# Kernel tuning notes

Hardware: AMD Instinct MI355X
Metric: run time of the kernel (lower is better)

## Reference

```python
import jax, jax.numpy as jnp
import numpy as np
import math

D_MODEL = 768
N_HEAD = 12
HEAD_DIM = D_MODEL // N_HEAD
B = 4
W = 32
HW = W * W


def setup_inputs() -> dict:
    key = jax.random.key(0)
    k1, k2, k3 = jax.random.split(key, 3)
    x = jax.random.normal(k1, (B, HW, D_MODEL), dtype=jnp.float32)
    w_qkv = jax.random.normal(k2, (3 * D_MODEL, D_MODEL), dtype=jnp.float32) * (D_MODEL ** -0.5)
    w_out = jax.random.normal(k3, (D_MODEL, D_MODEL), dtype=jnp.float32) * (D_MODEL ** -0.5)
    gamma = jnp.ones((D_MODEL,), dtype=jnp.float32)
    return {"x": x, "w_qkv": w_qkv, "w_out": w_out, "gamma": gamma}


def _axial_sincos(w, head_dim, dtype):
    # Axial RoPE: first half of head_dim encodes row position, second half column.
    dim_half = head_dim // 2
    inv_freq = 1.0 / (10000.0 ** (jnp.arange(0, dim_half, 2, dtype=dtype) / dim_half))  # (dim_half//2,)
    pos = jnp.arange(w, dtype=dtype)
    ang = pos[:, None] * inv_freq[None, :]                 # (w, f)
    row = jnp.repeat(ang[:, None, :], w, axis=1)           # (w, w, f)
    col = jnp.repeat(ang[None, :, :], w, axis=0)           # (w, w, f)
    theta = jnp.concatenate([row, col], axis=-1).reshape(w * w, dim_half)  # (hw, head_dim//2)
    theta = jnp.concatenate([theta, theta], axis=-1)       # rotate-half layout -> (hw, head_dim)
    return jnp.sin(theta), jnp.cos(theta)


def _rotate_half(t):
    t1, t2 = jnp.split(t, 2, axis=-1)
    return jnp.concatenate([-t2, t1], axis=-1)


def _apply_rotary(t, sin, cos):
    return t * cos + _rotate_half(t) * sin


def _rms_norm(x, gamma, eps=1e-6):
    return x * jax.lax.rsqrt(jnp.mean(x * x, axis=-1, keepdims=True) + eps) * gamma


def _attn_mask(w):
    # Faithful to the torch source: mask[center, neighbor] = False, else True.
    # torch SDPA bool semantics: True = attend. So 3x3 neighbors are EXCLUDED.
    idx = jnp.arange(w * w)
    r, c = idx // w, idx % w
    neighbor = (jnp.abs(r[:, None] - r[None, :]) <= 1) & (jnp.abs(c[:, None] - c[None, :]) <= 1)
    return ~neighbor  # (hw, hw) bool, True = allowed


def reference(x, w_qkv, w_out, gamma):
    Bx, hw, d = x.shape
    w = int(math.isqrt(hw))
    h, hd = N_HEAD, HEAD_DIM
    sin, cos = _axial_sincos(w, hd, x.dtype)               # (hw, hd) each
    xn = _rms_norm(x, gamma)
    qkv = xn @ w_qkv.T                                     # (B, hw, 3d)
    qkv = qkv.reshape(Bx, hw, 3, h, hd)
    q = jnp.transpose(qkv[:, :, 0], (0, 2, 1, 3))          # (B, h, hw, hd)
    k = jnp.transpose(qkv[:, :, 1], (0, 2, 1, 3))
    v = jnp.transpose(qkv[:, :, 2], (0, 2, 1, 3))
    q = _apply_rotary(q, sin, cos)
    k = _apply_rotary(k, sin, cos)
    allow = _attn_mask(w)
    scale = 1.0 / jnp.sqrt(jnp.asarray(hd, x.dtype))
    scores = jnp.einsum('bhid,bhjd->bhij', q, k) * scale   # (B, h, hw, hw)
    scores = jnp.where(allow[None, None], scores, jnp.asarray(-jnp.inf, x.dtype))
    probs = jax.nn.softmax(scores, axis=-1)
    out = jnp.einsum('bhij,bhjd->bhid', probs, v)          # (B, h, hw, hd)
    out = jnp.transpose(out, (0, 2, 1, 3)).reshape(Bx, hw, d)
    return out @ w_out.T
```

## Files before the change

### kernel.cpp

```cpp
#include <hip/hip_runtime.h>

typedef __attribute__((ext_vector_type(8))) short short8;
typedef __attribute__((ext_vector_type(4))) float f32x4;
typedef __attribute__((ext_vector_type(4))) unsigned short ushort4_t;
typedef unsigned short ushort_t;
typedef unsigned long long u64;

#define D_MODEL 768
#define NHEAD 12
#define HD 64
#define BATCH 4
#define HWIDTH 32
#define HW 1024
#define TOK (BATCH*HW)
#define QKV_N (3*D_MODEL)
#define BH (BATCH*NHEAD)
#define QSCALE 0.18033688f

__device__ __forceinline__ ushort_t f2bf(float f) {
    union { float f; unsigned u; } v; v.f = f;
    unsigned u = v.u;
    unsigned r = u + 0x7FFFu + ((u >> 16) & 1u);
    return (ushort_t)(r >> 16);
}
__device__ __forceinline__ float bf2f(ushort_t h) {
    union { unsigned u; float f; } v; v.u = ((unsigned)h) << 16;
    return v.f;
}
__device__ __forceinline__ float ex2(float x) {
    float r; asm("v_exp_f32 %0, %1" : "=v"(r) : "v"(x)); return r;
}
__device__ __forceinline__ unsigned cvtpk(float lo, float hi) {
    unsigned r; asm("v_cvt_pk_bf16_f32 %0, %1, %2" : "=v"(r) : "v"(lo), "v"(hi)); return r;
}

__global__ void rmsnorm_kernel(const float* __restrict__ x, const float* __restrict__ gamma,
                               ushort_t* __restrict__ xn) {
    int wave = threadIdx.x >> 6, lane = threadIdx.x & 63;
    int t = blockIdx.x * 4 + wave;
    const float* xr = x + (size_t)t * D_MODEL;
    float v[12]; float ss = 0.f;
    #pragma unroll
    for (int j = 0; j < 12; ++j) { v[j] = xr[lane + j*64]; ss += v[j]*v[j]; }
    #pragma unroll
    for (int m = 1; m < 64; m <<= 1) ss += __shfl_xor(ss, m, 64);
    float r = rsqrtf(ss * (1.f/768.f) + 1e-6f);
    ushort_t* o = xn + (size_t)t * D_MODEL;
    #pragma unroll
    for (int j = 0; j < 12; ++j) o[lane + j*64] = f2bf(v[j] * r * gamma[lane + j*64]);
}

__global__ void cvt_kernel(const float* __restrict__ in, ushort_t* __restrict__ out, int n) {
    int i = blockIdx.x * blockDim.x + threadIdx.x;
    if (i < n) out[i] = f2bf(in[i]);
}

__global__ void sincos_kernel(float* __restrict__ sint, float* __restrict__ cost) {
    int i = blockIdx.x * blockDim.x + threadIdx.x;
    int p = i >> 5, j = i & 31;
    int r = p >> 5, c = p & 31;
    int jj = j & 15;
    float freq = powf(10000.f, -(float)(2*jj) / 32.f);
    float pos = (j < 16) ? (float)r : (float)c;
    float th = pos * freq;
    sint[i] = sinf(th);
    cost[i] = cosf(th);
}

template<int NTILES, int EPI>
__global__ __launch_bounds__(256, 2) void gemm128(const ushort_t* __restrict__ A,
                                                  const ushort_t* __restrict__ B,
                                                  const float* __restrict__ sint,
                                                  const float* __restrict__ cost,
                                                  ushort_t* __restrict__ Qr,
                                                  ushort_t* __restrict__ Kr,
                                                  ushort_t* __restrict__ VTt,
                                                  float* __restrict__ C) {
    __shared__ ushort_t As[2][128*64];
    __shared__ ushort_t Bs[2][128*64];
    const int K = 768;
    constexpr int NR = NTILES / 2;
    int c = blockIdx.x & 7;
    int l = blockIdx.x >> 3;
    int mtile = (c >> 1)*8 + l / NR;
    int ntile = (c & 1)*NR + l % NR;
    int tm = mtile * 128, tn = ntile * 128;
    int w = threadIdx.x >> 6, lane = threadIdx.x & 63;
    int wr = w >> 1, wc = w & 1;
    int l15 = lane & 15, l4 = lane >> 4;

    const ushort_t* mat = (w < 2) ? A : B;
    int mbase = (w < 2) ? tm : tn;
    ushort_t* lds_half = (w < 2) ? &As[0][0] : &Bs[0][0];
    int r0w = (w & 1) * 64;
    int srow = r0w + (lane >> 3);
    int sslot = (lane & 7) ^ (srow & 7);
    const ushort_t* gsrc0 = mat + (size_t)(mbase + srow)*K + sslot*8;

    auto stage = [&](int buf, int kstep) {
        int k0 = kstep * 64;
        #pragma unroll
        for (int j = 0; j < 8; ++j) {
            const ushort_t* g = gsrc0 + (size_t)(j*8)*K + k0;
            __builtin_amdgcn_global_load_lds((const __attribute__((address_space(1))) void*)g,
                (__attribute__((address_space(3))) void*)(lds_half + (size_t)buf*8192 + (r0w + j*8)*64),
                16, 0, 0);
        }
    };

    f32x4 acc[4][4] = {};
    auto compute = [&](int bi) {
        short8 af[4][2], bfx[4][2];
        #pragma unroll
        for (int mi = 0; mi < 4; ++mi) {
            int row = wr*64 + mi*16 + l15;
            #pragma unroll
            for (int kk = 0; kk < 2; ++kk)
                af[mi][kk] = *(const short8*)&As[bi][row*64 + ((kk*4 + l4) ^ (row & 7))*8];
        }
        #pragma unroll
        for (int ni = 0; ni < 4; ++ni) {
            int row = wc*64 + ni*16 + l15;
            #pragma unroll
            for (int kk = 0; kk < 2; ++kk)
                bfx[ni][kk] = *(const short8*)&Bs[bi][row*64 + ((kk*4 + l4) ^ (row & 7))*8];
        }
        #pragma unroll
        for (int kk = 0; kk < 2; ++kk)
            #pragma unroll
            for (int mi = 0; mi < 4; ++mi)
                #pragma unroll
                for (int ni = 0; ni < 4; ++ni)
                    acc[mi][ni] = __builtin_amdgcn_mfma_f32_16x16x32_bf16(af[mi][kk], bfx[ni][kk], acc[mi][ni], 0, 0, 0);
    };

    stage(0, 0); stage(1, 1);
    for (int t = 0; t < 12; ++t) {
        if (t < 11) { asm volatile("s_waitcnt vmcnt(8)" ::: "memory"); }
        else        { asm volatile("s_waitcnt vmcnt(0)" ::: "memory"); }
        __builtin_amdgcn_s_barrier();
        compute(t & 1);
        __builtin_amdgcn_s_barrier();
        if (t < 10) stage(t & 1, t + 2);
    }

    if constexpr (EPI == 0) {
        int col_base = tn + wc*64;
        int region = col_base / 768;
        int h = (col_base % 768) >> 6;
        if (region < 2) {
            ushort_t* dst = (region == 0) ? Qr : Kr;
            float scale = (region == 0) ? QSCALE : 1.f;
            #pragma unroll
            for (int mi = 0; mi < 4; ++mi) {
                #pragma unroll
                for (int ni = 0; ni < 2; ++ni) {
                    int d = ni*16 + l15;
                    #pragma unroll
                    for (int r = 0; r < 4; ++r) {
                        int pt = tm + wr*64 + mi*16 + l4*4 + r;
                        int b = pt >> 10, p = pt & 1023;
                        float s = sint[p*32 + d], cc = cost[p*32 + d];
                        float t0 = acc[mi][ni][r], t1 = acc[mi][ni+2][r];
                        size_t o = (size_t)(b*NHEAD + h)*HW*HD + (size_t)p*HD + d;
                        dst[o]      = f2bf((t0*cc - t1*s) * scale);
                        dst[o + 32] = f2bf((t1*cc + t0*s) * scale);
                    }
                }
            }
        } else {
            #pragma unroll
            for (int mi = 0; mi < 4; ++mi) {
                int pt = tm + wr*64 + mi*16 + l4*4;
                int b = pt >> 10, p = pt & 1023;
                size_t hb = (size_t)(b*NHEAD + h)*HD*HW;
                #pragma unroll
                for (int ni = 0; ni < 4; ++ni) {
                    int d = ni*16 + l15;
                    ushort4_t pk;
                    pk.x = f2bf(acc[mi][ni][0]);
                    pk.y = f2bf(acc[mi][ni][1]);
                    pk.z = f2bf(acc[mi][ni][2]);
                    pk.w = f2bf(acc[mi][ni][3]);
                    *(ushort4_t*)&VTt[hb + (size_t)d*HW + p] = pk;
                }
            }
        }
    } else {
        #pragma unroll
        for (int mi = 0; mi < 4; ++mi)
            #pragma unroll
            for (int ni = 0; ni < 4; ++ni)
                #pragma unroll
                for (int r = 0; r < 4; ++r) {
                    int row = tm + wr*64 + mi*16 + l4*4 + r;
                    int col = tn + wc*64 + ni*16 + l15;
                    C[(size_t)row*(128*NTILES) + col] = acc[mi][ni][r];
                }
    }
}

__global__ __launch_bounds__(256) void attn_kernel(const ushort_t* __restrict__ Q,
                                                   const ushort_t* __restrict__ Kt,
                                                   const ushort_t* __restrict__ VT,
                                                   ushort_t* __restrict__ Ao) {
    __shared__ ushort_t Kb[2][64*64];
    __shared__ ushort_t Vb[2][64*64];
    __shared__ ushort_t P[4][16][72];
    int flat = blockIdx.x;
    int swz = (flat & 7) * 96 + (flat >> 3);
    int bh = swz >> 4;
    int qtile = swz & 15;
    int w = threadIdx.x >> 6, lane = threadIdx.x & 63;
    int l15 = lane & 15, l4 = lane >> 4;
    int qbase = qtile * 64 + w * 16;
    int q = qbase + l15;
    int qr = q >> 5, qc = q & 31;
    const ushort_t* Qh = Q + (size_t)bh * HW * HD;
    const ushort_t* Kh = Kt + (size_t)bh * HW * HD;
    const ushort_t* Vh = VT + (size_t)bh * HD * HW;
    short8 aq0 = *(const short8*)&Qh[(size_t)q*64 + l4*8];
    short8 aq1 = *(const short8*)&Qh[(size_t)q*64 + 32 + l4*8];
    unsigned pat = (qc == 0) ? 3u : (7u << (qc - 1));
    float m = -1e30f, lsum = 0.f;
    f32x4 oacc[4] = {};

    auto stage = [&](int bufi, int kv) {
        #pragma unroll
        for (int is = 0; is < 2; ++is) {
            int c = is*256 + w*64 + lane;
            int row = c >> 3;
            int col16 = (c & 7) ^ (row & 7);
            const ushort_t* ga = Kh + (size_t)(kv + row)*64 + col16*8;
            __builtin_amdgcn_global_load_lds((const __attribute__((address_space(1))) void*)ga,
                (__attribute__((address_space(3))) void*)(&Kb[bufi][(size_t)(is*256 + w*64)*8]), 16, 0, 0);
            const ushort_t* gv = Vh + (size_t)row*HW + kv + col16*8;
            __builtin_amdgcn_global_load_lds((const __attribute__((address_space(1))) void*)gv,
                (__attribute__((address_space(3))) void*)(&Vb[bufi][(size_t)(is*256 + w*64)*8]), 16, 0, 0);
        }
    };

    stage(0, 0); stage(1, 64);

    for (int t = 0; t < 16; ++t) {
        if (t < 15) { asm volatile("s_waitcnt vmcnt(4)" ::: "memory"); }
        else        { asm volatile("s_waitcnt vmcnt(0)" ::: "memory"); }
        __builtin_amdgcn_s_barrier();
        int cur = t & 1;
        int kv = t * 64;
        int sw = l15 & 7;
        f32x4 s[4];
        #pragma unroll
        for (int st = 0; st < 4; ++st) {
            int krow = st*16 + l15;
            short8 bk0 = *(const short8*)&Kb[cur][(size_t)krow*64 + (size_t)((l4 ^ sw))*8];
            short8 bk1 = *(const short8*)&Kb[cur][(size_t)krow*64 + (size_t)(((4+l4) ^ sw))*8];
            f32x4 z = {};
            z = __builtin_amdgcn_mfma_f32_16x16x32_bf16(bk0, aq0, z, 0, 0, 0);
            z = __builtin_amdgcn_mfma_f32_16x16x32_bf16(bk1, aq1, z, 0, 0, 0);
            s[st] = z;
        }
        short8 va0[4], va1[4];
        #pragma unroll
        for (int dt = 0; dt < 4; ++dt) {
            int vrow = dt*16 + l15;
            va0[dt] = *(const short8*)&Vb[cur][(size_t)vrow*64 + (size_t)((l4 ^ sw))*8];
            va1[dt] = *(const short8*)&Vb[cur][(size_t)vrow*64 + (size_t)(((4+l4) ^ sw))*8];
        }
        int dr = qr - (kv >> 5);
        if (dr >= -1 && dr <= 2) {
            u64 tm = 0;
            if (dr <= 1) tm |= (u64)pat;
            if (dr >= 0) tm |= ((u64)pat) << 32;
            u64 sub = tm >> (l4*4);
            #pragma unroll
            for (int st = 0; st < 4; ++st)
                #pragma unroll
                for (int i = 0; i < 4; ++i)
                    if ((sub >> (st*16 + i)) & 1) s[st][i] = -1e30f;
        }
        float vmax = fmaxf(
            fmaxf(fmaxf(fmaxf(s[0][0], s[0][1]), fmaxf(s[0][2], s[0][3])),
                  fmaxf(fmaxf(s[1][0], s[1][1]), fmaxf(s[1][2], s[1][3]))),
            fmaxf(fmaxf(fmaxf(s[2][0], s[2][1]), fmaxf(s[2][2], s[2][3])),
                  fmaxf(fmaxf(s[3][0], s[3][1]), fmaxf(s[3][2], s[3][3]))));
        vmax = fmaxf(vmax, __shfl_xor(vmax, 16, 64));
        vmax = fmaxf(vmax, __shfl_xor(vmax, 32, 64));
        if (__any(vmax - m > 8.f)) {
            float mn = fmaxf(m, vmax);
            float sf = ex2(m - mn);
            lsum *= sf;
            #pragma unroll
            for (int dt = 0; dt < 4; ++dt)
                #pragma unroll
                for (int i = 0; i < 4; ++i) oacc[dt][i] *= sf;
            m = mn;
        }
        float ls = 0.f;
        #pragma unroll
        for (int st = 0; st < 4; ++st) {
            float p0 = ex2(s[st][0] - m), p1 = ex2(s[st][1] - m);
            float p2 = ex2(s[st][2] - m), p3 = ex2(s[st][3] - m);
            ls += (p0 + p1) + (p2 + p3);
            uint2 pk;
            pk.x = cvtpk(p0, p1);
            pk.y = cvtpk(p2, p3);
            *(uint2*)&P[w][l15][st*16 + l4*4] = pk;
        }
        ls += __shfl_xor(ls, 16, 64);
        ls += __shfl_xor(ls, 32, 64);
        lsum += ls;
        short8 pf0 = *(const short8*)&P[w][l15][l4*8];
        short8 pf1 = *(const short8*)&P[w][l15][32 + l4*8];
        #pragma unroll
        for (int dt = 0; dt < 4; ++dt) {
            oacc[dt] = __builtin_amdgcn_mfma_f32_16x16x32_bf16(va0[dt], pf0, oacc[dt], 0, 0, 0);
            oacc[dt] = __builtin_amdgcn_mfma_f32_16x16x32_bf16(va1[dt], pf1, oacc[dt], 0, 0, 0);
        }
        __builtin_amdgcn_s_barrier();
        if (t < 14) stage(cur, (t + 2) * 64);
    }
    int b = bh / NHEAD, h = bh % NHEAD;
    float rl = 1.f / lsum;
    size_t obase = ((size_t)b*HW + q)*D_MODEL + h*64;
    #pragma unroll
    for (int dt = 0; dt < 4; ++dt) {
        uint2 pk;
        pk.x = cvtpk(oacc[dt][0]*rl, oacc[dt][1]*rl);
        pk.y = cvtpk(oacc[dt][2]*rl, oacc[dt][3]*rl);
        *(uint2*)&Ao[obase + dt*16 + l4*4] = pk;
    }
}

extern "C" void kernel_launch(void* const* d_in, const int* in_sizes, int n_in,
                              void* d_out, int out_size, void* d_ws, size_t ws_size,
                              hipStream_t stream) {
    const float* x      = (const float*)d_in[0];
    const float* w_qkv  = (const float*)d_in[1];
    const float* w_out  = (const float*)d_in[2];
    const float* gamma  = (const float*)d_in[3];
    float* out = (float*)d_out;

    char* ws = (char*)d_ws;
    size_t off = 0;
    auto alloc = [&](size_t bytes) { char* p = ws + off; off += (bytes + 255) & ~255ull; return p; };
    ushort_t* xn   = (ushort_t*)alloc((size_t)TOK*D_MODEL*2);
    ushort_t* wq   = (ushort_t*)alloc((size_t)QKV_N*D_MODEL*2);
    ushort_t* wo   = (ushort_t*)alloc((size_t)D_MODEL*D_MODEL*2);
    float* sint    = (float*)alloc((size_t)HW*32*4);
    float* cost    = (float*)alloc((size_t)HW*32*4);
    ushort_t* Qr   = (ushort_t*)alloc((size_t)BH*HW*HD*2);
    ushort_t* Kr   = (ushort_t*)alloc((size_t)BH*HW*HD*2);
    ushort_t* VTt  = (ushort_t*)alloc((size_t)BH*HD*HW*2);
    ushort_t* Ao   = (ushort_t*)alloc((size_t)TOK*D_MODEL*2);

    rmsnorm_kernel<<<TOK/4, 256, 0, stream>>>(x, gamma, xn);
    cvt_kernel<<<(QKV_N*D_MODEL + 255)/256, 256, 0, stream>>>(w_qkv, wq, QKV_N*D_MODEL);
    cvt_kernel<<<(D_MODEL*D_MODEL + 255)/256, 256, 0, stream>>>(w_out, wo, D_MODEL*D_MODEL);
    sincos_kernel<<<HW*32/256, 256, 0, stream>>>(sint, cost);
    gemm128<18,0><<<576, 256, 0, stream>>>(xn, wq, sint, cost, Qr, Kr, VTt, nullptr);
    attn_kernel<<<768, 256, 0, stream>>>(Qr, Kr, VTt, Ao);
    gemm128<6,1><<<192, 256, 0, stream>>>(Ao, wo, nullptr, nullptr, nullptr, nullptr, nullptr, out);
}
```

Measured before the change: 80.10 us.

## Fuse prep kernels and process two query tiles per wave in attention

Merges the RMSNorm, both weight conversions (now vectorized with float4 loads and packed bf16 stores) and the sin/cos table into one launch, cutting three kernel launches. The attention kernel now gives each wave 32 queries (two 16-row tiles) instead of 16, so each K/V tile staged into LDS feeds twice as many MFMAs. The grid is halved to 384 blocks. The cost is higher register pressure and fewer blocks to spread across the CUs, which may reduce occupancy and latency hiding.

```diff
diff --git a/kernel.cpp b/kernel.cpp
--- a/kernel.cpp
+++ b/kernel.cpp
@@ -23,10 +23,6 @@
     unsigned r = u + 0x7FFFu + ((u >> 16) & 1u);
     return (ushort_t)(r >> 16);
 }
-__device__ __forceinline__ float bf2f(ushort_t h) {
-    union { unsigned u; float f; } v; v.u = ((unsigned)h) << 16;
-    return v.f;
-}
 __device__ __forceinline__ float ex2(float x) {
     float r; asm("v_exp_f32 %0, %1" : "=v"(r) : "v"(x)); return r;
 }
@@ -34,37 +30,50 @@
     unsigned r; asm("v_cvt_pk_bf16_f32 %0, %1, %2" : "=v"(r) : "v"(lo), "v"(hi)); return r;
 }
 
-__global__ void rmsnorm_kernel(const float* __restrict__ x, const float* __restrict__ gamma,
-                               ushort_t* __restrict__ xn) {
-    int wave = threadIdx.x >> 6, lane = threadIdx.x & 63;
-    int t = blockIdx.x * 4 + wave;
-    const float* xr = x + (size_t)t * D_MODEL;
-    float v[12]; float ss = 0.f;
-    #pragma unroll
-    for (int j = 0; j < 12; ++j) { v[j] = xr[lane + j*64]; ss += v[j]*v[j]; }
-    #pragma unroll
-    for (int m = 1; m < 64; m <<= 1) ss += __shfl_xor(ss, m, 64);
-    float r = rsqrtf(ss * (1.f/768.f) + 1e-6f);
-    ushort_t* o = xn + (size_t)t * D_MODEL;
-    #pragma unroll
-    for (int j = 0; j < 12; ++j) o[lane + j*64] = f2bf(v[j] * r * gamma[lane + j*64]);
-}
-
-__global__ void cvt_kernel(const float* __restrict__ in, ushort_t* __restrict__ out, int n) {
-    int i = blockIdx.x * blockDim.x + threadIdx.x;
-    if (i < n) out[i] = f2bf(in[i]);
-}
-
-__global__ void sincos_kernel(float* __restrict__ sint, float* __restrict__ cost) {
-    int i = blockIdx.x * blockDim.x + threadIdx.x;
-    int p = i >> 5, j = i & 31;
-    int r = p >> 5, c = p & 31;
-    int jj = j & 15;
-    float freq = powf(10000.f, -(float)(2*jj) / 32.f);
-    float pos = (j < 16) ? (float)r : (float)c;
-    float th = pos * freq;
-    sint[i] = sinf(th);
-    cost[i] = cosf(th);
+__global__ __launch_bounds__(256) void prep_kernel(const float* __restrict__ x,
+                                                   const float* __restrict__ gamma,
+                                                   ushort_t* __restrict__ xn,
+                                                   const float* __restrict__ w_qkv,
+                                                   ushort_t* __restrict__ wq,
+                                                   const float* __restrict__ w_out,
+                                                   ushort_t* __restrict__ wo,
+                                                   float* __restrict__ sint,
+                                                   float* __restrict__ cost) {
+    int blk = blockIdx.x;
+    if (blk < 1024) {
+        int wave = threadIdx.x >> 6, lane = threadIdx.x & 63;
+        int t = blk * 4 + wave;
+        const float* xr = x + (size_t)t * D_MODEL;
+        float v[12]; float ss = 0.f;
+        #pragma unroll
+        for (int j = 0; j < 12; ++j) { v[j] = xr[lane + j*64]; ss += v[j]*v[j]; }
+        #pragma unroll
+        for (int m = 1; m < 64; m <<= 1) ss += __shfl_xor(ss, m, 64);
+        float r = rsqrtf(ss * (1.f/768.f) + 1e-6f);
+        ushort_t* o = xn + (size_t)t * D_MODEL;
+        #pragma unroll
+        for (int j = 0; j < 12; ++j) o[lane + j*64] = f2bf(v[j] * r * gamma[lane + j*64]);
+    } else if (blk < 2752) {
+        int i = (blk - 1024) * 1024 + threadIdx.x * 4;
+        float4 v = *(const float4*)&w_qkv[i];
+        uint2 pk; pk.x = cvtpk(v.x, v.y); pk.y = cvtpk(v.z, v.w);
+        *(uint2*)&wq[i] = pk;
+    } else if (blk < 3328) {
+        int i = (blk - 2752) * 1024 + threadIdx.x * 4;
+        float4 v = *(const float4*)&w_out[i];
+        uint2 pk; pk.x = cvtpk(v.x, v.y); pk.y = cvtpk(v.z, v.w);
+        *(uint2*)&wo[i] = pk;
+    } else {
+        int i = (blk - 3328) * 256 + threadIdx.x;
+        int p = i >> 5, j = i & 31;
+        int r = p >> 5, c = p & 31;
+        int jj = j & 15;
+        float freq = powf(10000.f, -(float)(2*jj) / 32.f);
+        float pos = (j < 16) ? (float)r : (float)c;
+        float th = pos * freq;
+        sint[i] = sinf(th);
+        cost[i] = cosf(th);
+    }
 }
 
 template<int NTILES, int EPI>
@@ -206,24 +215,27 @@
                                                    ushort_t* __restrict__ Ao) {
     __shared__ ushort_t Kb[2][64*64];
     __shared__ ushort_t Vb[2][64*64];
-    __shared__ ushort_t P[4][16][72];
+    __shared__ ushort_t P[4][32][72];
     int flat = blockIdx.x;
-    int swz = (flat & 7) * 96 + (flat >> 3);
-    int bh = swz >> 4;
-    int qtile = swz & 15;
+    int swz = (flat & 7) * 48 + (flat >> 3);
+    int bh = swz >> 3;
+    int qtile = swz & 7;
     int w = threadIdx.x >> 6, lane = threadIdx.x & 63;
     int l15 = lane & 15, l4 = lane >> 4;
-    int qbase = qtile * 64 + w * 16;
-    int q = qbase + l15;
-    int qr = q >> 5, qc = q & 31;
+    int qbase = qtile * 128 + w * 32;
+    int q0 = qbase + l15, q1 = q0 + 16;
+    int qr = qbase >> 5;
     const ushort_t* Qh = Q + (size_t)bh * HW * HD;
     const ushort_t* Kh = Kt + (size_t)bh * HW * HD;
     const ushort_t* Vh = VT + (size_t)bh * HD * HW;
-    short8 aq0 = *(const short8*)&Qh[(size_t)q*64 + l4*8];
-    short8 aq1 = *(const short8*)&Qh[(size_t)q*64 + 32 + l4*8];
-    unsigned pat = (qc == 0) ? 3u : (7u << (qc - 1));
-    float m = -1e30f, lsum = 0.f;
-    f32x4 oacc[4] = {};
+    short8 aq0_0 = *(const short8*)&Qh[(size_t)q0*64 + l4*8];
+    short8 aq1_0 = *(const short8*)&Qh[(size_t)q0*64 + 32 + l4*8];
+    short8 aq0_1 = *(const short8*)&Qh[(size_t)q1*64 + l4*8];
+    short8 aq1_1 = *(const short8*)&Qh[(size_t)q1*64 + 32 + l4*8];
+    unsigned pat0 = (l15 == 0) ? 3u : (7u << (l15 - 1));
+    unsigned pat1 = 7u << (l15 + 15);
+    float m0 = -1e30f, ls0 = 0.f, m1 = -1e30f, ls1 = 0.f;
+    f32x4 oacc0[4] = {}, oacc1[4] = {};
 
     auto stage = [&](int bufi, int kv) {
         #pragma unroll
@@ -249,16 +261,18 @@
         int cur = t & 1;
         int kv = t * 64;
         int sw = l15 & 7;
-        f32x4 s[4];
+        f32x4 s0[4], s1[4];
         #pragma unroll
         for (int st = 0; st < 4; ++st) {
             int krow = st*16 + l15;
             short8 bk0 = *(const short8*)&Kb[cur][(size_t)krow*64 + (size_t)((l4 ^ sw))*8];
             short8 bk1 = *(const short8*)&Kb[cur][(size_t)krow*64 + (size_t)(((4+l4) ^ sw))*8];
-            f32x4 z = {};
-            z = __builtin_amdgcn_mfma_f32_16x16x32_bf16(bk0, aq0, z, 0, 0, 0);
-            z = __builtin_amdgcn_mfma_f32_16x16x32_bf16(bk1, aq1, z, 0, 0, 0);
-            s[st] = z;
+            f32x4 z0 = {}, z1 = {};
+            z0 = __builtin_amdgcn_mfma_f32_16x16x32_bf16(bk0, aq0_0, z0, 0, 0, 0);
+            z0 = __builtin_amdgcn_mfma_f32_16x16x32_bf16(bk1, aq1_0, z0, 0, 0, 0);
+            z1 = __builtin_amdgcn_mfma_f32_16x16x32_bf16(bk0, aq0_1, z1, 0, 0, 0);
+            z1 = __builtin_amdgcn_mfma_f32_16x16x32_bf16(bk1, aq1_1, z1, 0, 0, 0);
+            s0[st] = z0; s1[st] = z1;
         }
         short8 va0[4], va1[4];
         #pragma unroll
@@ -269,66 +283,107 @@
         }
         int dr = qr - (kv >> 5);
         if (dr >= -1 && dr <= 2) {
-            u64 tm = 0;
-            if (dr <= 1) tm |= (u64)pat;
-            if (dr >= 0) tm |= ((u64)pat) << 32;
-            u64 sub = tm >> (l4*4);
+            u64 tm0 = 0, tm1 = 0;
+            if (dr <= 1) { tm0 |= (u64)pat0; tm1 |= (u64)pat1; }
+            if (dr >= 0) { tm0 |= ((u64)pat0) << 32; tm1 |= ((u64)pat1) << 32; }
+            u64 sub0 = tm0 >> (l4*4), sub1 = tm1 >> (l4*4);
             #pragma unroll
             for (int st = 0; st < 4; ++st)
                 #pragma unroll
-                for (int i = 0; i < 4; ++i)
-                    if ((sub >> (st*16 + i)) & 1) s[st][i] = -1e30f;
-        }
-        float vmax = fmaxf(
-            fmaxf(fmaxf(fmaxf(s[0][0], s[0][1]), fmaxf(s[0][2], s[0][3])),
-                  fmaxf(fmaxf(s[1][0], s[1][1]), fmaxf(s[1][2], s[1][3]))),
-            fmaxf(fmaxf(fmaxf(s[2][0], s[2][1]), fmaxf(s[2][2], s[2][3])),
-                  fmaxf(fmaxf(s[3][0], s[3][1]), fmaxf(s[3][2], s[3][3]))));
-        vmax = fmaxf(vmax, __shfl_xor(vmax, 16, 64));
-        vmax = fmaxf(vmax, __shfl_xor(vmax, 32, 64));
-        if (__any(vmax - m > 8.f)) {
-            float mn = fmaxf(m, vmax);
-            float sf = ex2(m - mn);
-            lsum *= sf;
-            #pragma unroll
-            for (int dt = 0; dt < 4; ++dt)
-                #pragma unroll
-                for (int i = 0; i < 4; ++i) oacc[dt][i] *= sf;
-            m = mn;
-        }
-        float ls = 0.f;
-        #pragma unroll
-        for (int st = 0; st < 4; ++st) {
-            float p0 = ex2(s[st][0] - m), p1 = ex2(s[st][1] - m);
-            float p2 = ex2(s[st][2] - m), p3 = ex2(s[st][3] - m);
-            ls += (p0 + p1) + (p2 + p3);
-            uint2 pk;
-            pk.x = cvtpk(p0, p1);
-            pk.y = cvtpk(p2, p3);
-            *(uint2*)&P[w][l15][st*16 + l4*4] = pk;
-        }
-        ls += __shfl_xor(ls, 16, 64);
-        ls += __shfl_xor(ls, 32, 64);
-        lsum += ls;
-        short8 pf0 = *(const short8*)&P[w][l15][l4*8];
-        short8 pf1 = *(const short8*)&P[w][l15][32 + l4*8];
+                for (int i = 0; i < 4; ++i) {
+                    if ((sub0 >> (st*16 + i)) & 1) s0[st][i] = -1e30f;
+                    if ((sub1 >> (st*16 + i)) & 1) s1[st][i] = -1e30f;
+                }
+        }
+        {
+            float vmax = fmaxf(
+                fmaxf(fmaxf(fmaxf(s0[0][0], s0[0][1]), fmaxf(s0[0][2], s0[0][3])),
+                      fmaxf(fmaxf(s0[1][0], s0[1][1]), fmaxf(s0[1][2], s0[1][3]))),
+                fmaxf(fmaxf(fmaxf(s0[2][0], s0[2][1]), fmaxf(s0[2][2], s0[2][3])),
+                      fmaxf(fmaxf(s0[3][0], s0[3][1]), fmaxf(s0[3][2], s0[3][3]))));
+            vmax = fmaxf(vmax, __shfl_xor(vmax, 16, 64));
+            vmax = fmaxf(vmax, __shfl_xor(vmax, 32, 64));
+            if (__any(vmax - m0 > 8.f)) {
+                float mn = fmaxf(m0, vmax);
+                float sf = ex2(m0 - mn);
+                ls0 *= sf;
+                #pragma unroll
+                for (int dt = 0; dt < 4; ++dt)
+                    #pragma unroll
+                    for (int i = 0; i < 4; ++i) oacc0[dt][i] *= sf;
+                m0 = mn;
+            }
+            float ls = 0.f;
+            #pragma unroll
+            for (int st = 0; st < 4; ++st) {
+                float p0 = ex2(s0[st][0] - m0), p1 = ex2(s0[st][1] - m0);
+                float p2 = ex2(s0[st][2] - m0), p3 = ex2(s0[st][3] - m0);
+                ls += (p0 + p1) + (p2 + p3);
+                uint2 pk; pk.x = cvtpk(p0, p1); pk.y = cvtpk(p2, p3);
+                *(uint2*)&P[w][l15][st*16 + l4*4] = pk;
+            }
+            ls += __shfl_xor(ls, 16, 64);
+            ls += __shfl_xor(ls, 32, 64);
+            ls0 += ls;
+        }
+        {
+            float vmax = fmaxf(
+                fmaxf(fmaxf(fmaxf(s1[0][0], s1[0][1]), fmaxf(s1[0][2], s1[0][3])),
+                      fmaxf(fmaxf(s1[1][0], s1[1][1]), fmaxf(s1[1][2], s1[1][3]))),
+                fmaxf(fmaxf(fmaxf(s1[2][0], s1[2][1]), fmaxf(s1[2][2], s1[2][3])),
+                      fmaxf(fmaxf(s1[3][0], s1[3][1]), fmaxf(s1[3][2], s1[3][3]))));
+            vmax = fmaxf(vmax, __shfl_xor(vmax, 16, 64));
+            vmax = fmaxf(vmax, __shfl_xor(vmax, 32, 64));
+            if (__any(vmax - m1 > 8.f)) {
+                float mn = fmaxf(m1, vmax);
+                float sf = ex2(m1 - mn);
+                ls1 *= sf;
+                #pragma unroll
+                for (int dt = 0; dt < 4; ++dt)
+                    #pragma unroll
+                    for (int i = 0; i < 4; ++i) oacc1[dt][i] *= sf;
+                m1 = mn;
+            }
+            float ls = 0.f;
+            #pragma unroll
+            for (int st = 0; st < 4; ++st) {
+                float p0 = ex2(s1[st][0] - m1), p1 = ex2(s1[st][1] - m1);
+                float p2 = ex2(s1[st][2] - m1), p3 = ex2(s1[st][3] - m1);
+                ls += (p0 + p1) + (p2 + p3);
+                uint2 pk; pk.x = cvtpk(p0, p1); pk.y = cvtpk(p2, p3);
+                *(uint2*)&P[w][16 + l15][st*16 + l4*4] = pk;
+            }
+            ls += __shfl_xor(ls, 16, 64);
+            ls += __shfl_xor(ls, 32, 64);
+            ls1 += ls;
+        }
+        short8 pf0_0 = *(const short8*)&P[w][l15][l4*8];
+        short8 pf1_0 = *(const short8*)&P[w][l15][32 + l4*8];
+        short8 pf0_1 = *(const short8*)&P[w][16 + l15][l4*8];
+        short8 pf1_1 = *(const short8*)&P[w][16 + l15][32 + l4*8];
         #pragma unroll
         for (int dt = 0; dt < 4; ++dt) {
-            oacc[dt] = __builtin_amdgcn_mfma_f32_16x16x32_bf16(va0[dt], pf0, oacc[dt], 0, 0, 0);
-            oacc[dt] = __builtin_amdgcn_mfma_f32_16x16x32_bf16(va1[dt], pf1, oacc[dt], 0, 0, 0);
+            oacc0[dt] = __builtin_amdgcn_mfma_f32_16x16x32_bf16(va0[dt], pf0_0, oacc0[dt], 0, 0, 0);
+            oacc0[dt] = __builtin_amdgcn_mfma_f32_16x16x32_bf16(va1[dt], pf1_0, oacc0[dt], 0, 0, 0);
+            oacc1[dt] = __builtin_amdgcn_mfma_f32_16x16x32_bf16(va0[dt], pf0_1, oacc1[dt], 0, 0, 0);
+            oacc1[dt] = __builtin_amdgcn_mfma_f32_16x16x32_bf16(va1[dt], pf1_1, oacc1[dt], 0, 0, 0);
         }
         __builtin_amdgcn_s_barrier();
         if (t < 14) stage(cur, (t + 2) * 64);
     }
     int b = bh / NHEAD, h = bh % NHEAD;
-    float rl = 1.f / lsum;
-    size_t obase = ((size_t)b*HW + q)*D_MODEL + h*64;
+    float rl0 = 1.f / ls0, rl1 = 1.f / ls1;
+    size_t ob0 = ((size_t)b*HW + q0)*D_MODEL + h*64;
+    size_t ob1 = ((size_t)b*HW + q1)*D_MODEL + h*64;
     #pragma unroll
     for (int dt = 0; dt < 4; ++dt) {
-        uint2 pk;
-        pk.x = cvtpk(oacc[dt][0]*rl, oacc[dt][1]*rl);
-        pk.y = cvtpk(oacc[dt][2]*rl, oacc[dt][3]*rl);
-        *(uint2*)&Ao[obase + dt*16 + l4*4] = pk;
+        uint2 pk0, pk1;
+        pk0.x = cvtpk(oacc0[dt][0]*rl0, oacc0[dt][1]*rl0);
+        pk0.y = cvtpk(oacc0[dt][2]*rl0, oacc0[dt][3]*rl0);
+        pk1.x = cvtpk(oacc1[dt][0]*rl1, oacc1[dt][1]*rl1);
+        pk1.y = cvtpk(oacc1[dt][2]*rl1, oacc1[dt][3]*rl1);
+        *(uint2*)&Ao[ob0 + dt*16 + l4*4] = pk0;
+        *(uint2*)&Ao[ob1 + dt*16 + l4*4] = pk1;
     }
 }
 
@@ -354,11 +409,8 @@
     ushort_t* VTt  = (ushort_t*)alloc((size_t)BH*HD*HW*2);
     ushort_t* Ao   = (ushort_t*)alloc((size_t)TOK*D_MODEL*2);
 
-    rmsnorm_kernel<<<TOK/4, 256, 0, stream>>>(x, gamma, xn);
-    cvt_kernel<<<(QKV_N*D_MODEL + 255)/256, 256, 0, stream>>>(w_qkv, wq, QKV_N*D_MODEL);
-    cvt_kernel<<<(D_MODEL*D_MODEL + 255)/256, 256, 0, stream>>>(w_out, wo, D_MODEL*D_MODEL);
-    sincos_kernel<<<HW*32/256, 256, 0, stream>>>(sint, cost);
+    prep_kernel<<<3456, 256, 0, stream>>>(x, gamma, xn, w_qkv, wq, w_out, wo, sint, cost);
     gemm128<18,0><<<576, 256, 0, stream>>>(xn, wq, sint, cost, Qr, Kr, VTt, nullptr);
-    attn_kernel<<<768, 256, 0, stream>>>(Qr, Kr, VTt, Ao);
+    attn_kernel<<<384, 256, 0, stream>>>(Qr, Kr, VTt, Ao);
     gemm128<6,1><<<192, 256, 0, stream>>>(Ao, wo, nullptr, nullptr, nullptr, nullptr, nullptr, out);
 }
```

New measurement: 77.51 us. -3.2%, faster.
